# Optimization experiments

Hardware: AMD Instinct MI355X
Metric: run time of the kernel (lower is better)

Reference implementation:

```python
import jax, jax.numpy as jnp
import numpy as np

# Mesh/packing dims: deltaV_packed.view(B, M, V, ndims) requires N = B*M*V
B, M, V = 2, 4, 40000
N = B * M * V            # 320_000 packed vertices
E = 960000               # ~3 edges per vertex (triangle mesh)
F_IN = 128               # n_input_features
LAT = 128                # latent_channels
NDIMS = 3
N_HIDDEN = 2             # n_f2f_hidden_layer


def graph_conv(x, edges, W0, b0, W1, b1):
    """pytorch3d-style GraphConv: w0(x) + sum_{j in N(i)} w1(x_j), undirected edges."""
    h0 = x @ W0 + b0                     # self term  [N, out]
    h1 = x @ W1 + b1                     # neighbor messages [N, out]
    src, dst = edges[:, 0], edges[:, 1]
    agg = jnp.zeros_like(h0).at[src].add(h1[dst]).at[dst].add(h1[src])
    return h0 + agg


def setup_inputs() -> dict:
    key = jax.random.key(0)
    ks = jax.random.split(key, 20)
    inp = {
        "features": jax.random.normal(ks[0], (N, F_IN), jnp.float32),
        "edges": jax.random.randint(ks[1], (E, 2), 0, N, dtype=jnp.int32),
    }
    # Layer dims: f2f first (F_IN->LAT), 2 hidden (LAT->LAT), f2v (LAT->NDIMS).
    dims = [(F_IN, LAT), (LAT, LAT), (LAT, LAT), (LAT, NDIMS)]
    for i, (din, dout) in enumerate(dims):
        kk = jax.random.split(ks[2 + i], 4)
        s = 1.0 / np.sqrt(din)
        inp[f"W0_{i}"] = jax.random.normal(kk[0], (din, dout), jnp.float32) * s
        inp[f"b0_{i}"] = jnp.zeros((dout,), jnp.float32)
        inp[f"W1_{i}"] = jax.random.normal(kk[1], (din, dout), jnp.float32) * s
        inp[f"b1_{i}"] = jnp.zeros((dout,), jnp.float32)
    return inp


def reference(features, edges,
              W0_0, b0_0, W1_0, b1_0,
              W0_1, b0_1, W1_1, b1_1,
              W0_2, b0_2, W1_2, b1_2,
              W0_3, b0_3, W1_3, b1_3):
    # Features2FeaturesResidual: first GC + 2 hidden GCs (ReLU each, norm='none'),
    # residual skip (identity since F_IN == LAT).
    h = jax.nn.relu(graph_conv(features, edges, W0_0, b0_0, W1_0, b1_0))
    h = jax.nn.relu(graph_conv(h, edges, W0_1, b0_1, W1_1, b1_1))
    h = jax.nn.relu(graph_conv(h, edges, W0_2, b0_2, W1_2, b1_2))
    h = h + features
    # f2v: GC(latent -> ndims), no activation
    deltaV = graph_conv(h, edges, W0_3, b0_3, W1_3, b1_3)
    return deltaV.reshape(B, M, V, NDIMS)
```

## Files before the change

### kernel.cpp

```cpp
#include <hip/hip_runtime.h>
#include <hip/hip_bf16.h>

#define NNODES 320000
#define NEDGES 960000
#define NPART 8
#define PARTSZ (NNODES / NPART)

typedef __attribute__((ext_vector_type(8))) short short8;
typedef __attribute__((ext_vector_type(4))) float f32x4;

__device__ __forceinline__ float b2f(unsigned short u) {
    return __uint_as_float(((unsigned)u) << 16);
}
__device__ __forceinline__ unsigned short f2b(float f) {
    __hip_bfloat16 h = __float2bfloat16(f);
    union { __hip_bfloat16 h; unsigned short u; } cv;
    cv.h = h;
    return cv.u;
}


__global__ void k_zero(int* p, int n) {
    int i = blockIdx.x * blockDim.x + threadIdx.x;
    int s = gridDim.x * blockDim.x;
    for (; i < n; i += s) p[i] = 0;
}

__global__ void k_count(const int* __restrict__ edges, int* __restrict__ deg) {
    int r = blockIdx.x & (NPART - 1);
    int lo = r * PARTSZ, hi = lo + PARTSZ;
    int i = (blockIdx.x >> 3) * blockDim.x + threadIdx.x;
    int s = (gridDim.x >> 3) * blockDim.x;
    for (; i < NEDGES; i += s) {
        int2 e = *(const int2*)&edges[2 * i];
        if (e.x >= lo && e.x < hi) atomicAdd(&deg[e.x], 1);
        if (e.y >= lo && e.y < hi) atomicAdd(&deg[e.y], 1);
    }
}

#define SCAN_BLOCK 256
#define SCAN_ITEMS 8
#define SCAN_CHUNK 2048
#define SCAN_NB 157

__global__ void k_scan1(const int* __restrict__ deg, int* __restrict__ bsum) {
    __shared__ int sd[SCAN_BLOCK];
    int b = blockIdx.x, t = threadIdx.x;
    int base = b * SCAN_CHUNK + t * SCAN_ITEMS;
    int s = 0;
    for (int i = 0; i < SCAN_ITEMS; i++) {
        int g = base + i;
        if (g < NNODES) s += deg[g];
    }
    sd[t] = s;
    __syncthreads();
    for (int off = 128; off > 0; off >>= 1) {
        if (t < off) sd[t] += sd[t + off];
        __syncthreads();
    }
    if (t == 0) bsum[b] = sd[0];
}

__global__ void k_scan2(int* bsum, int* rowptr) {
    __shared__ int sd[256];
    int t = threadIdx.x;
    int v = (t < SCAN_NB) ? bsum[t] : 0;
    sd[t] = v;
    __syncthreads();
    for (int off = 1; off < 256; off <<= 1) {
        int x = (t >= off) ? sd[t - off] : 0;
        __syncthreads();
        sd[t] += x;
        __syncthreads();
    }
    if (t < SCAN_NB) bsum[t] = sd[t] - v;
    if (t == SCAN_NB - 1) rowptr[NNODES] = sd[t];
}

__global__ void k_scan3(int* __restrict__ deg_cursor, int* __restrict__ rowptr,
                        const int* __restrict__ bsum, float* __restrict__ degf) {
    __shared__ int sd[SCAN_BLOCK];
    int b = blockIdx.x, t = threadIdx.x;
    int base = b * SCAN_CHUNK + t * SCAN_ITEMS;
    int v[SCAN_ITEMS];
    int s = 0;
    for (int i = 0; i < SCAN_ITEMS; i++) {
        int g = base + i;
        v[i] = (g < NNODES) ? deg_cursor[g] : 0;
        s += v[i];
    }
    sd[t] = s;
    __syncthreads();
    for (int off = 1; off < SCAN_BLOCK; off <<= 1) {
        int x = (t >= off) ? sd[t - off] : 0;
        __syncthreads();
        sd[t] += x;
        __syncthreads();
    }
    int prefix = bsum[b] + (sd[t] - s);
    for (int i = 0; i < SCAN_ITEMS; i++) {
        int g = base + i;
        if (g < NNODES) {
            rowptr[g] = prefix;
            deg_cursor[g] = prefix;
            degf[g] = (float)v[i];
            prefix += v[i];
        }
    }
}

__global__ void k_fill(const int* __restrict__ edges, int* __restrict__ cursor,
                       int* __restrict__ adj) {
    int r = blockIdx.x & (NPART - 1);
    int lo = r * PARTSZ, hi = lo + PARTSZ;
    int i = (blockIdx.x >> 3) * blockDim.x + threadIdx.x;
    int s = (gridDim.x >> 3) * blockDim.x;
    for (; i < NEDGES; i += s) {
        int2 e = *(const int2*)&edges[2 * i];
        if (e.x >= lo && e.x < hi) adj[atomicAdd(&cursor[e.x], 1)] = e.y;
        if (e.y >= lo && e.y < hi) adj[atomicAdd(&cursor[e.y], 1)] = e.x;
    }
}


__global__ void k_cvt(const float* __restrict__ f, unsigned short* __restrict__ o,
                      long n4) {
    long i = (long)blockIdx.x * blockDim.x + threadIdx.x;
    long s = (long)gridDim.x * blockDim.x;
    for (; i < n4; i += s) {
        float4 v = *(const float4*)&f[i * 4];
        uint2 u;
        u.x = (unsigned)f2b(v.x) | ((unsigned)f2b(v.y) << 16);
        u.y = (unsigned)f2b(v.z) | ((unsigned)f2b(v.w) << 16);
        *(uint2*)&o[i * 4] = u;
    }
}

__global__ void k_cvtW(const float* __restrict__ W0, const float* __restrict__ W1,
                       unsigned short* __restrict__ Wt) {
    int idx = blockIdx.x * blockDim.x + threadIdx.x;
    if (idx >= 128 * 256) return;
    int c = idx >> 8, k = idx & 255;
    float v = (k < 128) ? W0[k * 128 + c] : W1[(k - 128) * 128 + c];
    Wt[idx] = f2b(v);
}


template <int L>
__global__ __launch_bounds__(256) void k_gather(
    const unsigned short* __restrict__ x, const int* __restrict__ rowptr,
    const int* __restrict__ adj, unsigned short* __restrict__ xsum) {
    int wid = (blockIdx.x * blockDim.x + threadIdx.x) >> 6;
    int lane = threadIdx.x & 63;
    int nw = (gridDim.x * blockDim.x) >> 6;
    int slot = lane >> 4;
    int cb = (lane & 15) * 8;
    for (int n0 = wid * 2; n0 < NNODES; n0 += nw * 2) {
        int s0 = rowptr[n0], e0 = rowptr[n0 + 1], e1 = rowptr[n0 + 2];
        int d0 = e0 - s0, d1 = e1 - e0;
        int dmax = d0 > d1 ? d0 : d1;
        float a0[8], a1[8];
#pragma unroll
        for (int q = 0; q < 8; q++) { a0[q] = 0.f; a1[q] = 0.f; }
        for (int p = 0; p < dmax; p += 8) {
            int i00 = s0 + p + slot, i01 = i00 + 4;
            int i10 = e0 + p + slot, i11 = i10 + 4;
            uint4 v00 = make_uint4(0, 0, 0, 0), v01 = make_uint4(0, 0, 0, 0);
            uint4 v10 = make_uint4(0, 0, 0, 0), v11 = make_uint4(0, 0, 0, 0);
            if (i00 < e0) v00 = *(const uint4*)&x[(size_t)adj[i00] * 128 + cb];
            if (i01 < e0) v01 = *(const uint4*)&x[(size_t)adj[i01] * 128 + cb];
            if (i10 < e1) v10 = *(const uint4*)&x[(size_t)adj[i10] * 128 + cb];
            if (i11 < e1) v11 = *(const uint4*)&x[(size_t)adj[i11] * 128 + cb];
            unsigned w00[4] = {v00.x, v00.y, v00.z, v00.w};
            unsigned w01[4] = {v01.x, v01.y, v01.z, v01.w};
            unsigned w10[4] = {v10.x, v10.y, v10.z, v10.w};
            unsigned w11[4] = {v11.x, v11.y, v11.z, v11.w};
#pragma unroll
            for (int q = 0; q < 4; q++) {
                a0[2 * q] += b2f(w00[q] & 0xffff) + b2f(w01[q] & 0xffff);
                a0[2 * q + 1] += b2f(w00[q] >> 16) + b2f(w01[q] >> 16);
                a1[2 * q] += b2f(w10[q] & 0xffff) + b2f(w11[q] & 0xffff);
                a1[2 * q + 1] += b2f(w10[q] >> 16) + b2f(w11[q] >> 16);
            }
        }
#pragma unroll
        for (int q = 0; q < 8; q++) {
            a0[q] += __shfl_xor(a0[q], 16, 64);
            a1[q] += __shfl_xor(a1[q], 16, 64);
        }
#pragma unroll
        for (int q = 0; q < 8; q++) {
            a0[q] += __shfl_xor(a0[q], 32, 64);
            a1[q] += __shfl_xor(a1[q], 32, 64);
        }
        float sel[8];
#pragma unroll
        for (int q = 0; q < 8; q++) sel[q] = (lane < 16) ? a0[q] : a1[q];
        if (lane < 32) {
            uint4 o;
            o.x = (unsigned)f2b(sel[0]) | ((unsigned)f2b(sel[1]) << 16);
            o.y = (unsigned)f2b(sel[2]) | ((unsigned)f2b(sel[3]) << 16);
            o.z = (unsigned)f2b(sel[4]) | ((unsigned)f2b(sel[5]) << 16);
            o.w = (unsigned)f2b(sel[6]) | ((unsigned)f2b(sel[7]) << 16);
            int dst = (lane < 16) ? n0 : (n0 + 1);
            *(uint4*)&xsum[(size_t)dst * 128 + cb] = o;
        }
    }
}


#define XLD 136
#define NT (NNODES / 64)

template <int RES, int L>
__global__ __launch_bounds__(512, 2) void k_gemmF(
    const unsigned short* x, const unsigned short* __restrict__ xsum,
    const unsigned short* __restrict__ Wt, const float* __restrict__ b0,
    const float* __restrict__ b1, const float* __restrict__ degf,
    const unsigned short* __restrict__ feat, unsigned short* out) {
    __shared__ __align__(16) unsigned short Xs[64 * XLD];
    __shared__ __align__(16) unsigned short Ss[64 * XLD];

    int tid = threadIdx.x;
    int wave = tid >> 6, lane = tid & 63;
    int wm = wave >> 2, wn = wave & 3;
    int kg = (lane >> 4) << 3;
    int cl = lane & 15;

    float bias0[2], bias1[2];
#pragma unroll
    for (int nf = 0; nf < 2; nf++) {
        int c = wn * 32 + nf * 16 + cl;
        bias0[nf] = b0[c];
        bias1[nf] = b1[c];
    }

    uint4 pa[2], ps[2];
    auto loadTile = [&](int tile) {
#pragma unroll
        for (int it = 0; it < 2; ++it) {
            int e = (it * 512 + tid) * 8;
            int r = e >> 7, k = e & 127;
            pa[it] = *(const uint4*)&x[(size_t)(tile * 64 + r) * 128 + k];
            ps[it] = *(const uint4*)&xsum[(size_t)(tile * 64 + r) * 128 + k];
        }
    };

    int tile = blockIdx.x;
    if (tile < NT) loadTile(tile);
    while (tile < NT) {
        int next = tile + gridDim.x;
        __syncthreads();
#pragma unroll
        for (int it = 0; it < 2; ++it) {
            int e = (it * 512 + tid) * 8;
            int r = e >> 7, k = e & 127;
            *(uint4*)&Xs[r * XLD + k] = pa[it];
            *(uint4*)&Ss[r * XLD + k] = ps[it];
        }
        __syncthreads();
        if (next < NT) loadTile(next);

        int rowBase = tile * 64;
        f32x4 acc[2][2];
#pragma unroll
        for (int i = 0; i < 2; i++)
#pragma unroll
            for (int j = 0; j < 2; j++) acc[i][j] = (f32x4){0.f, 0.f, 0.f, 0.f};

#pragma unroll
        for (int ks = 0; ks < 8; ++ks) {
            const unsigned short* src = (ks < 4) ? Xs : Ss;
            int kk = (ks & 3) * 32 + kg;
            short8 aF[2];
#pragma unroll
            for (int mf = 0; mf < 2; ++mf) {
                int r = wm * 32 + mf * 16 + cl;
                aF[mf] = *(const short8*)&src[r * XLD + kk];
            }
#pragma unroll
            for (int nf = 0; nf < 2; nf++) {
                int c = wn * 32 + nf * 16 + cl;
                short8 bF = *(const short8*)&Wt[(size_t)c * 256 + ks * 32 + kg];
#pragma unroll
                for (int mf = 0; mf < 2; mf++)
                    acc[mf][nf] = __builtin_amdgcn_mfma_f32_16x16x32_bf16(
                        aF[mf], bF, acc[mf][nf], 0, 0, 0);
            }
        }

#pragma unroll
        for (int nf = 0; nf < 2; nf++) {
            int c = wn * 32 + nf * 16 + cl;
#pragma unroll
            for (int mf = 0; mf < 2; mf++) {
                int r0 = rowBase + wm * 32 + mf * 16 + ((lane >> 4) << 2);
                f32x4 d = acc[mf][nf];
#pragma unroll
                for (int q = 0; q < 4; q++) {
                    int r = r0 + q;
                    float v = d[q] + bias0[nf] + degf[r] * bias1[nf];
                    v = fmaxf(v, 0.f);
                    if (RES) v += b2f(feat[(size_t)r * 128 + c]);
                    out[(size_t)r * 128 + c] = f2b(v);
                }
            }
        }
        tile = next;
    }
}


__global__ __launch_bounds__(256) void k_fin(
    const unsigned short* __restrict__ act, const unsigned short* __restrict__ hsum,
    const float* __restrict__ W0, const float* __restrict__ W1,
    const float* __restrict__ b0, const float* __restrict__ b1,
    const float* __restrict__ degf, float* __restrict__ out) {
    __shared__ __align__(16) unsigned short xa[64 * XLD];
    __shared__ __align__(16) unsigned short xs2[64 * XLD];
    __shared__ float Wf[768];
    __shared__ float ps[64][4][4];

    int tid = threadIdx.x;
    int nodeBase = blockIdx.x * 64;

    for (int idx = tid; idx < 384; idx += 256) {
        Wf[idx] = W0[idx];
        Wf[384 + idx] = W1[idx];
    }
#pragma unroll
    for (int it = 0; it < 4; ++it) {
        int e = (it * 256 + tid) * 8;
        int r = e >> 7, k = e & 127;
        *(uint4*)&xa[r * XLD + k] = *(const uint4*)&act[(size_t)(nodeBase + r) * 128 + k];
        *(uint4*)&xs2[r * XLD + k] =
            *(const uint4*)&hsum[(size_t)(nodeBase + r) * 128 + k];
    }
    __syncthreads();

    int n = tid >> 2, q = tid & 3;
    const unsigned short* src = (q < 2) ? xa : xs2;
    int kloc = (q & 1) * 64;
    float a0 = 0.f, a1 = 0.f, a2 = 0.f;
#pragma unroll
    for (int kk = 0; kk < 64; kk += 8) {
        uint4 v = *(const uint4*)&src[n * XLD + kloc + kk];
        unsigned vv[4] = {v.x, v.y, v.z, v.w};
#pragma unroll
        for (int t = 0; t < 4; t++) {
            int kgl = q * 64 + kk + 2 * t;
            float x0 = b2f(vv[t] & 0xffff), x1 = b2f(vv[t] >> 16);
            const float* w = &Wf[kgl * 3];
            a0 += x0 * w[0] + x1 * w[3];
            a1 += x0 * w[1] + x1 * w[4];
            a2 += x0 * w[2] + x1 * w[5];
        }
    }
    ps[n][q][0] = a0;
    ps[n][q][1] = a1;
    ps[n][q][2] = a2;
    __syncthreads();
    if (q == 0) {
        int node = nodeBase + n;
        float dg = degf[node];
#pragma unroll
        for (int c = 0; c < 3; c++) {
            float d = ps[n][0][c] + ps[n][1][c] + ps[n][2][c] + ps[n][3][c] +
                      b0[c] + dg * b1[c];
            out[(size_t)node * 3 + c] = d;
        }
    }
}


extern "C" void kernel_launch(void* const* d_in, const int* in_sizes, int n_in,
                              void* d_out, int out_size, void* d_ws, size_t ws_size,
                              hipStream_t stream) {
    const float* features = (const float*)d_in[0];
    const int* edges = (const int*)d_in[1];
    const float *W0[4], *B0[4], *W1[4], *B1[4];
    for (int i = 0; i < 4; i++) {
        W0[i] = (const float*)d_in[2 + 4 * i];
        B0[i] = (const float*)d_in[3 + 4 * i];
        W1[i] = (const float*)d_in[4 + 4 * i];
        B1[i] = (const float*)d_in[5 + 4 * i];
    }

    char* p = (char*)d_ws;
    auto alloc = [&](size_t bytes) {
        void* r = (void*)p;
        p += (bytes + 255) & ~(size_t)255;
        return r;
    };
    int* rowptr = (int*)alloc((NNODES + 1) * sizeof(int));
    int* cursor = (int*)alloc((NNODES + 1) * sizeof(int));
    float* degf = (float*)alloc(NNODES * sizeof(float));
    int* adj = (int*)alloc((size_t)2 * NEDGES * sizeof(int));
    int* bsum = (int*)alloc(1024);
    unsigned short* feat_bf = (unsigned short*)alloc((size_t)NNODES * 128 * 2);
    unsigned short* act = (unsigned short*)alloc((size_t)NNODES * 128 * 2);
    unsigned short* xsum = (unsigned short*)alloc((size_t)NNODES * 128 * 2);
    unsigned short* Wtb = (unsigned short*)alloc((size_t)3 * 128 * 256 * 2);

    k_zero<<<1024, 256, 0, stream>>>(cursor, NNODES + 1);
    k_count<<<2048, 256, 0, stream>>>(edges, cursor);
    k_scan1<<<SCAN_NB, SCAN_BLOCK, 0, stream>>>(cursor, bsum);
    k_scan2<<<1, 256, 0, stream>>>(bsum, rowptr);
    k_scan3<<<SCAN_NB, SCAN_BLOCK, 0, stream>>>(cursor, rowptr, bsum, degf);
    k_fill<<<2048, 256, 0, stream>>>(edges, cursor, adj);

    k_cvt<<<2048, 256, 0, stream>>>(features, feat_bf, (long)NNODES * 128 / 4);
    for (int l = 0; l < 3; l++)
        k_cvtW<<<128, 256, 0, stream>>>(W0[l], W1[l], Wtb + (size_t)l * 128 * 256);

    k_gather<0><<<8192, 256, 0, stream>>>(feat_bf, rowptr, adj, xsum);
    k_gemmF<0, 0><<<1250, 512, 0, stream>>>(feat_bf, xsum, Wtb, B0[0], B1[0], degf,
                                            nullptr, act);
    k_gather<1><<<8192, 256, 0, stream>>>(act, rowptr, adj, xsum);
    k_gemmF<0, 1><<<1250, 512, 0, stream>>>(act, xsum, Wtb + 128 * 256, B0[1], B1[1],
                                            degf, nullptr, act);
    k_gather<2><<<8192, 256, 0, stream>>>(act, rowptr, adj, xsum);
    k_gemmF<1, 2><<<1250, 512, 0, stream>>>(act, xsum, Wtb + 2 * 128 * 256, B0[2],
                                            B1[2], degf, feat_bf, act);
    k_gather<3><<<8192, 256, 0, stream>>>(act, rowptr, adj, xsum);
    k_fin<<<NNODES / 64, 256, 0, stream>>>(act, xsum, W0[3], W1[3], B0[3], B1[3],
                                           degf, (float*)d_out);
}
```

Baseline: 1.169 ms.

## Project final layer to 3 dims before neighbor aggregation; raise gemm occupancy hint

The last graph conv now multiplies each node's 128-dim activation by W0 and W1 first, storing 3+3 floats per node. Aggregation then gathers only the small W1-projected vectors instead of full 128-wide bf16 rows, which removes the fourth full-width gather and its xsum traffic. The gemm kernel's launch bounds also change from 2 to 4 blocks per SM, which may force register spills. The final output's summation order changes slightly, and the projected buffer reuses the xsum workspace.

Result: faster. 1.089 ms (-6.8%).

```diff
diff --git a/kernel.cpp b/kernel.cpp
--- a/kernel.cpp
+++ b/kernel.cpp
@@ -213,7 +213,7 @@
 #define NT (NNODES / 64)
 
 template <int RES, int L>
-__global__ __launch_bounds__(512, 2) void k_gemmF(
+__global__ __launch_bounds__(512, 4) void k_gemmF(
     const unsigned short* x, const unsigned short* __restrict__ xsum,
     const unsigned short* __restrict__ Wt, const float* __restrict__ b0,
     const float* __restrict__ b1, const float* __restrict__ degf,
@@ -311,64 +311,83 @@
 }
 
 
-__global__ __launch_bounds__(256) void k_fin(
-    const unsigned short* __restrict__ act, const unsigned short* __restrict__ hsum,
-    const float* __restrict__ W0, const float* __restrict__ W1,
-    const float* __restrict__ b0, const float* __restrict__ b1,
-    const float* __restrict__ degf, float* __restrict__ out) {
-    __shared__ __align__(16) unsigned short xa[64 * XLD];
-    __shared__ __align__(16) unsigned short xs2[64 * XLD];
-    __shared__ float Wf[768];
-    __shared__ float ps[64][4][4];
-
+#define LDK3 136
+
+__global__ __launch_bounds__(256) void k_fin3(
+    const unsigned short* __restrict__ act, const float* __restrict__ W0p,
+    const float* __restrict__ W1p, float* __restrict__ h3) {
+    __shared__ __align__(16) unsigned short xs[128 * LDK3];
+    __shared__ float Ws[128 * 8];
     int tid = threadIdx.x;
-    int nodeBase = blockIdx.x * 64;
+    int nodeBase = blockIdx.x * 128;
 
     for (int idx = tid; idx < 384; idx += 256) {
-        Wf[idx] = W0[idx];
-        Wf[384 + idx] = W1[idx];
-    }
-#pragma unroll
-    for (int it = 0; it < 4; ++it) {
+        int k = idx / 3, c = idx - k * 3;
+        Ws[k * 8 + c] = W0p[idx];
+        Ws[k * 8 + 4 + c] = W1p[idx];
+    }
+    for (int it = 0; it < 8; ++it) {
         int e = (it * 256 + tid) * 8;
-        int r = e >> 7, k = e & 127;
-        *(uint4*)&xa[r * XLD + k] = *(const uint4*)&act[(size_t)(nodeBase + r) * 128 + k];
-        *(uint4*)&xs2[r * XLD + k] =
-            *(const uint4*)&hsum[(size_t)(nodeBase + r) * 128 + k];
+        int r = e >> 7;
+        int k = e & 127;
+        *(uint4*)&xs[r * LDK3 + k] = *(const uint4*)&act[(size_t)(nodeBase + r) * 128 + k];
     }
     __syncthreads();
 
-    int n = tid >> 2, q = tid & 3;
-    const unsigned short* src = (q < 2) ? xa : xs2;
-    int kloc = (q & 1) * 64;
+    int n = tid >> 1, half = tid & 1;
     float a0 = 0.f, a1 = 0.f, a2 = 0.f;
 #pragma unroll
-    for (int kk = 0; kk < 64; kk += 8) {
-        uint4 v = *(const uint4*)&src[n * XLD + kloc + kk];
+    for (int k0 = 0; k0 < 128; k0 += 8) {
+        uint4 v = *(const uint4*)&xs[n * LDK3 + k0];
         unsigned vv[4] = {v.x, v.y, v.z, v.w};
 #pragma unroll
-        for (int t = 0; t < 4; t++) {
-            int kgl = q * 64 + kk + 2 * t;
-            float x0 = b2f(vv[t] & 0xffff), x1 = b2f(vv[t] >> 16);
-            const float* w = &Wf[kgl * 3];
-            a0 += x0 * w[0] + x1 * w[3];
-            a1 += x0 * w[1] + x1 * w[4];
-            a2 += x0 * w[2] + x1 * w[5];
-        }
-    }
-    ps[n][q][0] = a0;
-    ps[n][q][1] = a1;
-    ps[n][q][2] = a2;
-    __syncthreads();
-    if (q == 0) {
-        int node = nodeBase + n;
+        for (int q = 0; q < 4; q++) {
+            int k = k0 + 2 * q;
+            float x0 = b2f(vv[q] & 0xffff), x1 = b2f(vv[q] >> 16);
+            const float* w = &Ws[k * 8 + half * 4];
+            a0 += x0 * w[0] + x1 * w[8];
+            a1 += x0 * w[1] + x1 * w[9];
+            a2 += x0 * w[2] + x1 * w[10];
+        }
+    }
+    float* dst = &h3[(size_t)(nodeBase + n) * 8 + half * 4];
+    dst[0] = a0;
+    dst[1] = a1;
+    dst[2] = a2;
+}
+
+
+__global__ void k_agg3(const float* __restrict__ h3, const int* __restrict__ rowptr,
+                       const int* __restrict__ adj, const float* __restrict__ b0,
+                       const float* __restrict__ b1, const float* __restrict__ degf,
+                       float* __restrict__ out) {
+    int i = blockIdx.x * blockDim.x + threadIdx.x;
+    int stride = gridDim.x * blockDim.x;
+    for (int node = i; node < NNODES; node += stride) {
+        float4 dv = *(const float4*)&h3[(size_t)node * 8];
         float dg = degf[node];
-#pragma unroll
-        for (int c = 0; c < 3; c++) {
-            float d = ps[n][0][c] + ps[n][1][c] + ps[n][2][c] + ps[n][3][c] +
-                      b0[c] + dg * b1[c];
-            out[(size_t)node * 3 + c] = d;
-        }
+        float a0 = dv.x + b0[0] + dg * b1[0];
+        float a1 = dv.y + b0[1] + dg * b1[1];
+        float a2 = dv.z + b0[2] + dg * b1[2];
+        int s = rowptr[node], e = rowptr[node + 1];
+        int p = s;
+        for (; p + 2 <= e; p += 2) {
+            int j0 = adj[p], j1 = adj[p + 1];
+            float4 v0 = *(const float4*)&h3[(size_t)j0 * 8 + 4];
+            float4 v1 = *(const float4*)&h3[(size_t)j1 * 8 + 4];
+            a0 += v0.x + v1.x;
+            a1 += v0.y + v1.y;
+            a2 += v0.z + v1.z;
+        }
+        if (p < e) {
+            float4 v = *(const float4*)&h3[(size_t)adj[p] * 8 + 4];
+            a0 += v.x;
+            a1 += v.y;
+            a2 += v.z;
+        }
+        out[(size_t)node * 3 + 0] = a0;
+        out[(size_t)node * 3 + 1] = a1;
+        out[(size_t)node * 3 + 2] = a2;
     }
 }
 
@@ -401,6 +420,7 @@
     unsigned short* act = (unsigned short*)alloc((size_t)NNODES * 128 * 2);
     unsigned short* xsum = (unsigned short*)alloc((size_t)NNODES * 128 * 2);
     unsigned short* Wtb = (unsigned short*)alloc((size_t)3 * 128 * 256 * 2);
+    float* h3 = (float*)xsum;
 
     k_zero<<<1024, 256, 0, stream>>>(cursor, NNODES + 1);
     k_count<<<2048, 256, 0, stream>>>(edges, cursor);
@@ -422,7 +442,7 @@
     k_gather<2><<<8192, 256, 0, stream>>>(act, rowptr, adj, xsum);
     k_gemmF<1, 2><<<1250, 512, 0, stream>>>(act, xsum, Wtb + 2 * 128 * 256, B0[2],
                                             B1[2], degf, feat_bf, act);
-    k_gather<3><<<8192, 256, 0, stream>>>(act, rowptr, adj, xsum);
-    k_fin<<<NNODES / 64, 256, 0, stream>>>(act, xsum, W0[3], W1[3], B0[3], B1[3],
-                                           degf, (float*)d_out);
-}
+    k_fin3<<<NNODES / 128, 256, 0, stream>>>(act, W0[3], W1[3], h3);
+    k_agg3<<<2048, 256, 0, stream>>>(h3, rowptr, adj, B0[3], B1[3], degf,
+                                     (float*)d_out);
+}
```
